# Optimization experiments

Measured on AMD Instinct MI355X. Metric: run time of the kernel, lower is better.

The kernel has to match this reference:

```python
import jax, jax.numpy as jnp
import numpy as np
from jax import lax

B, L, D = 2, 2048, 128
H, HD = 8, 32
WIN = 3

def setup_inputs() -> dict:
    key = jax.random.key(0)
    ks = jax.random.split(key, 7)
    s = 0.05
    return {
        "x":  jax.random.normal(ks[0], (B, L, D), jnp.float32),
        "pe": jax.random.normal(ks[1], (L, D), jnp.float32) * s,
        "Wq": jax.random.normal(ks[2], (D, H * HD), jnp.float32) * s,
        "bq": jnp.zeros((H * HD,), jnp.float32),
        "Wk": jax.random.normal(ks[3], (D, H * HD), jnp.float32) * s,
        "bk": jnp.zeros((H * HD,), jnp.float32),
        "Wv": jax.random.normal(ks[4], (D, H), jnp.float32) * s,
    }

def reference(x, pe, Wq, bq, Wk, bk, Wv):
    b, l, d = x.shape
    h = Wv.shape[1]
    hd = Wq.shape[1] // h
    xp = x + pe                                   # (B,L,D)
    # split heads: Dense output columns [i*hd:(i+1)*hd] -> head i
    q = (xp @ Wq + bq).reshape(b, l, h, hd).transpose(2, 0, 1, 3)  # (H,B,L,hd)
    k = (xp @ Wk + bk).reshape(b, l, h, hd).transpose(2, 0, 1, 3)  # (H,B,L,hd)
    v = jax.nn.sigmoid(x @ Wv).transpose(2, 0, 1)                  # (H,B,L)

    attn = jnp.einsum('hbqd,hbkd->hbqk', q, k) * (float(hd) ** -0.5)
    attn = jax.nn.softmax(attn, axis=-1)          # (H,B,L,L)

    # band_part(0,-1) + diag_part(k=(0,L-1)) (RIGHT_LEFT align) + transpose + reverse(-2,-1)
    # collapses to the skew-gather: R[p, m] = attn[L-1-p-m, L-1-p] for p+m <= L-1 else 0
    p = jnp.arange(l)[:, None]                    # (L,1)
    m = jnp.arange(l)[None, :]                    # (1,L)
    ii = l - 1 - p - m                            # row index  (L,L)
    jj = jnp.broadcast_to(l - 1 - p, (l, l))      # col index  (L,L)
    valid = (ii >= 0)
    R = attn[:, :, jnp.where(valid, ii, 0), jj] * valid.astype(attn.dtype)  # (H,B,L,L)

    R = R * v[:, :, :, None]                      # gate by value, broadcast over distance axis

    # TF avg_pool excludes padding from the divisor
    sums = lax.reduce_window(R, 0.0, lax.add, (1, 1, 1, WIN), (1, 1, 1, 1), 'SAME')
    cnt = lax.reduce_window(jnp.ones((l,), R.dtype), 0.0, lax.add, (WIN,), (1,), 'SAME')
    pooled = sums / cnt                           # (H,B,L,L)

    # global mode: sum over position axis, -> (B, L_dist, H)
    out = pooled.sum(axis=2).transpose(1, 2, 0)
    return out
```

## Files before the change

kernel.cpp:

```cpp
#include <hip/hip_runtime.h>
#include <hip/hip_bf16.h>

#define LSEQ 2048
#define BB 2
#define DD 128
#define HH 8
#define HD 32

#define FPSCALE 524288.0f
#define RFPSCALE (1.0f / 524288.0f)
#define DENSCALE 65536.0f
#define QSCALE 0.25503486f

typedef __bf16 bf8_t __attribute__((ext_vector_type(8)));
typedef __bf16 bf4_t __attribute__((ext_vector_type(4)));
typedef float f4_t __attribute__((ext_vector_type(4)));

__global__ __launch_bounds__(256) void k_A(const float* __restrict__ x,
                                           const float* __restrict__ pe,
                                           const float* __restrict__ Wq,
                                           const float* __restrict__ Wk,
                                           const float* __restrict__ Wv,
                                           const float* __restrict__ bq,
                                           const float* __restrict__ bk,
                                           float* __restrict__ w,
                                           __bf16* __restrict__ Qb,
                                           __bf16* __restrict__ Kb,
                                           int* __restrict__ Si,
                                           int* __restrict__ denI) {
    __shared__ __align__(16) char smem[34816];
    int gb = blockIdx.x;
    int tid = threadIdx.x;

    if (gb < 512) {
        __bf16* xs = (__bf16*)smem;
        __bf16* Wt = (__bf16*)(smem + 64 * 136 * 2);
        int jr = gb >> 3, y = gb & 7;
        int row0 = jr * 64;
        bool isK = y >= 4;
        int cbase = (y & 3) * 64;
        const float* W = isK ? Wk : Wq;

        #pragma unroll
        for (int i = 0; i < 8; i++) {
            int idx4 = tid + i * 256;
            int row = idx4 >> 5, col4 = idx4 & 31;
            float4 xv = ((const float4*)x)[row0 * 32 + idx4];
            float4 pv = ((const float4*)pe)[((row0 + row) & (LSEQ - 1)) * 32 + col4];
            bf4_t o = {(__bf16)(xv.x + pv.x), (__bf16)(xv.y + pv.y),
                       (__bf16)(xv.z + pv.z), (__bf16)(xv.w + pv.w)};
            *(bf4_t*)&xs[row * 136 + col4 * 4] = o;
        }
        #pragma unroll
        for (int i = 0; i < 8; i++) {
            int idx4 = tid + i * 256;
            int d = idx4 >> 4, c4 = (idx4 & 15) * 4;
            float4 wv4 = *(const float4*)(W + d * 256 + cbase + c4);
            Wt[(c4 + 0) * 136 + d] = (__bf16)wv4.x;
            Wt[(c4 + 1) * 136 + d] = (__bf16)wv4.y;
            Wt[(c4 + 2) * 136 + d] = (__bf16)wv4.z;
            Wt[(c4 + 3) * 136 + d] = (__bf16)wv4.w;
        }
        __syncthreads();

        int wid = tid >> 6, lane = tid & 63;
        int lm = lane & 15, lq = lane >> 4;
        int c0loc = wid * 16;
        f4_t acc0 = {0,0,0,0}, acc1 = {0,0,0,0}, acc2 = {0,0,0,0}, acc3 = {0,0,0,0};
        #pragma unroll
        for (int s = 0; s < 4; s++) {
            bf8_t bw = *(const bf8_t*)&Wt[(c0loc + lm) * 136 + lq * 8 + s * 32];
            bf8_t a0 = *(const bf8_t*)&xs[(0  + lm) * 136 + lq * 8 + s * 32];
            bf8_t a1 = *(const bf8_t*)&xs[(16 + lm) * 136 + lq * 8 + s * 32];
            bf8_t a2 = *(const bf8_t*)&xs[(32 + lm) * 136 + lq * 8 + s * 32];
            bf8_t a3 = *(const bf8_t*)&xs[(48 + lm) * 136 + lq * 8 + s * 32];
            acc0 = __builtin_amdgcn_mfma_f32_16x16x32_bf16(a0, bw, acc0, 0, 0, 0);
            acc1 = __builtin_amdgcn_mfma_f32_16x16x32_bf16(a1, bw, acc1, 0, 0, 0);
            acc2 = __builtin_amdgcn_mfma_f32_16x16x32_bf16(a2, bw, acc2, 0, 0, 0);
            acc3 = __builtin_amdgcn_mfma_f32_16x16x32_bf16(a3, bw, acc3, 0, 0, 0);
        }
        int c = cbase + c0loc + lm;
        float bv = (isK ? bk : bq)[c];
        float qs = isK ? 1.f : QSCALE;
        __bf16* Out = isK ? Kb : Qb;
        int h = c >> 5, hd = c & 31;
        f4_t accs[4] = {acc0, acc1, acc2, acc3};
        #pragma unroll
        for (int rs = 0; rs < 4; rs++) {
            #pragma unroll
            for (int r = 0; r < 4; r++) {
                int row = row0 + rs * 16 + lq * 4 + r;
                int b_ = row >> 11, l = row & (LSEQ - 1);
                Out[((h * BB + b_) * LSEQ + l) * HD + hd] =
                    (__bf16)((accs[rs][r] + bv) * qs);
            }
        }
    } else if (gb < 640) {
        float* xsf = (float*)smem;
        float* wvf = (float*)(smem + 32 * 132 * 4);
        int r0 = (gb - 512) * 32;
        for (int i = 0; i < 16; i++) {
            int idx = tid + i * 256;
            xsf[(idx >> 7) * 132 + (idx & 127)] = x[r0 * 128 + idx];
        }
        for (int i = 0; i < 4; i++) {
            int idx = tid + i * 256;
            wvf[idx] = Wv[idx];
        }
        __syncthreads();
        int rl = tid >> 3, h = tid & 7;
        float acc = 0.f;
        #pragma unroll 8
        for (int d = 0; d < 128; d++) acc += xsf[rl * 132 + d] * wvf[d * 8 + h];
        float sg = 1.f / (1.f + __expf(-acc));
        int r = r0 + rl;
        int b = r >> 11, l = r & (LSEQ - 1);
        w[(h * BB + b) * LSEQ + (LSEQ - 1 - l)] = sg;
    } else if (gb < 672) {
        int4 z = {0, 0, 0, 0};
        ((int4*)Si)[(gb - 640) * 256 + tid] = z;
    } else {
        int4 z = {0, 0, 0, 0};
        ((int4*)denI)[(gb - 672) * 256 + tid] = z;
    }
}

__global__ __launch_bounds__(256) void k_den(const __bf16* __restrict__ Qb,
                                             const __bf16* __restrict__ Kb,
                                             int* __restrict__ denI) {
    int hb = blockIdx.z;
    int q0 = blockIdx.y * 128;
    int kbase = blockIdx.x * 512;
    int wid = threadIdx.x >> 6, lane = threadIdx.x & 63;
    int lm = lane & 15, lq = lane >> 4;
    int qa = q0 + wid * 16;
    int qb2 = qa + 64;

    bf8_t aqa = *(const bf8_t*)(Qb + (hb * LSEQ + qa + lm) * HD + lq * 8);
    bf8_t aqb = *(const bf8_t*)(Qb + (hb * LSEQ + qb2 + lm) * HD + lq * 8);
    const __bf16* Khb = Kb + hb * LSEQ * HD;

    float dsa[4] = {0.f, 0.f, 0.f, 0.f};
    float dsb[4] = {0.f, 0.f, 0.f, 0.f};
    #pragma unroll 4
    for (int s = 0; s < 32; s++) {
        bf8_t bk_ = *(const bf8_t*)(Khb + (kbase + s * 16 + lm) * HD + lq * 8);
        f4_t z = {0.f, 0.f, 0.f, 0.f};
        f4_t sa = __builtin_amdgcn_mfma_f32_16x16x32_bf16(aqa, bk_, z, 0, 0, 0);
        f4_t sb = __builtin_amdgcn_mfma_f32_16x16x32_bf16(aqb, bk_, z, 0, 0, 0);
        #pragma unroll
        for (int r = 0; r < 4; r++) { dsa[r] += exp2f(sa[r]); dsb[r] += exp2f(sb[r]); }
    }
    #pragma unroll
    for (int r = 0; r < 4; r++) {
        float va = dsa[r], vb = dsb[r];
        va += __shfl_xor(va, 1); vb += __shfl_xor(vb, 1);
        va += __shfl_xor(va, 2); vb += __shfl_xor(vb, 2);
        va += __shfl_xor(va, 4); vb += __shfl_xor(vb, 4);
        va += __shfl_xor(va, 8); vb += __shfl_xor(vb, 8);
        dsa[r] = va; dsb[r] = vb;
    }
    if (lm == 0) {
        #pragma unroll
        for (int r = 0; r < 4; r++) {
            atomicAdd(&denI[hb * LSEQ + qa + lq * 4 + r],
                      __float2int_rn(dsa[r] * DENSCALE));
            atomicAdd(&denI[hb * LSEQ + qb2 + lq * 4 + r],
                      __float2int_rn(dsb[r] * DENSCALE));
        }
    }
}

#define SSTRIDE 332
__global__ __launch_bounds__(256) void k_scat(const __bf16* __restrict__ Qb,
                                              const __bf16* __restrict__ Kb,
                                              const float* __restrict__ w,
                                              const int* __restrict__ denI,
                                              int* __restrict__ S) {
    int hb = blockIdx.z;
    int q0 = blockIdx.y * 64;
    int kc0 = blockIdx.x * 256;
    if (kc0 + 256 <= q0) return;

    __shared__ int Sloc[16 * SSTRIDE];
    __shared__ float lwt[256];
    int tid = threadIdx.x;
    for (int i = tid; i < 16 * SSTRIDE; i += 256) Sloc[i] = 0;
    lwt[tid] = log2f(w[hb * LSEQ + kc0 + tid]);

    int wid = tid >> 6, lane = tid & 63;
    int lm = lane & 15, lq = lane >> 4;
    int qw0 = q0 + wid * 16;
    bf8_t aq = *(const bf8_t*)(Qb + (hb * LSEQ + qw0 + lm) * HD + lq * 8);
    float lrd[4];
    #pragma unroll
    for (int r = 0; r < 4; r++)
        lrd[r] = log2f(DENSCALE * FPSCALE / (float)denI[hb * LSEQ + qw0 + lq * 4 + r]);
    __syncthreads();

    const __bf16* Khb = Kb + hb * LSEQ * HD;
    int mbase = kc0 - q0 - 63;
    int qrow = qw0 + lq * 4;
    int* mySloc = Sloc + (wid * 4 + lq) * SSTRIDE;

    int sub_start = (qw0 > kc0) ? ((qw0 - kc0) >> 4) : 0;

    {
        int k0s = kc0 + sub_start * 16;
        bf8_t bk_ = *(const bf8_t*)(Khb + (k0s + lm) * HD + lq * 8);
        f4_t z = {0.f, 0.f, 0.f, 0.f};
        f4_t sc = __builtin_amdgcn_mfma_f32_16x16x32_bf16(aq, bk_, z, 0, 0, 0);
        float lw = lwt[sub_start * 16 + lm];
        int kcol = k0s + lm;
        #pragma unroll
        for (int r = 0; r < 4; r++) {
            int m = kcol - (qrow + r);
            if (m >= 0) {
                int iv = __float2int_rn(exp2f(sc[r] + lrd[r] + lw));
                atomicAdd(&mySloc[m - mbase], iv);
            }
        }
    }
    #pragma unroll 4
    for (int sub = sub_start + 1; sub < 16; sub++) {
        int k0s = kc0 + sub * 16;
        bf8_t bk_ = *(const bf8_t*)(Khb + (k0s + lm) * HD + lq * 8);
        f4_t z = {0.f, 0.f, 0.f, 0.f};
        f4_t sc = __builtin_amdgcn_mfma_f32_16x16x32_bf16(aq, bk_, z, 0, 0, 0);
        float lw = lwt[sub * 16 + lm];
        int kcol = k0s + lm;
        #pragma unroll
        for (int r = 0; r < 4; r++) {
            int m = kcol - (qrow + r);
            int iv = __float2int_rn(exp2f(sc[r] + lrd[r] + lw));
            atomicAdd(&mySloc[m - mbase], iv);
        }
    }
    __syncthreads();
    for (int i = tid; i < 320; i += 256) {
        int m = mbase + i;
        int v = 0;
        #pragma unroll
        for (int s = 0; s < 16; s++) v += Sloc[s * SSTRIDE + i];
        if (m >= 0 && m < LSEQ && v != 0)
            atomicAdd(&S[hb * LSEQ + m], v);
    }
}

__global__ __launch_bounds__(256) void k_out(const int* __restrict__ S,
                                             float* __restrict__ out) {
    int idx = blockIdx.x * 256 + threadIdx.x;
    int h = idx & 7;
    int m = (idx >> 3) & (LSEQ - 1);
    int b = idx >> 14;
    const int* Sr = S + (h * BB + b) * LSEQ;
    float s = (float)Sr[m];
    float cnt = 3.f;
    if (m > 0) s += (float)Sr[m - 1]; else cnt = 2.f;
    if (m < LSEQ - 1) s += (float)Sr[m + 1]; else cnt = 2.f;
    out[idx] = s * RFPSCALE / cnt;
}

extern "C" void kernel_launch(void* const* d_in, const int* in_sizes, int n_in,
                              void* d_out, int out_size, void* d_ws, size_t ws_size,
                              hipStream_t stream) {
    const float* x  = (const float*)d_in[0];
    const float* pe = (const float*)d_in[1];
    const float* Wq = (const float*)d_in[2];
    const float* bq = (const float*)d_in[3];
    const float* Wk = (const float*)d_in[4];
    const float* bk = (const float*)d_in[5];
    const float* Wv = (const float*)d_in[6];
    float* out = (float*)d_out;

    char* ws = (char*)d_ws;
    int*    Si   = (int*)(ws);
    float*  w    = (float*)(ws + 131072);
    __bf16* Qb   = (__bf16*)(ws + 262144);
    __bf16* Kb   = (__bf16*)(ws + 262144 + 2097152);
    int*    denI = (int*)(ws + 262144 + 4194304);

    k_A<<<704, 256, 0, stream>>>(x, pe, Wq, Wk, Wv, bq, bk, w, Qb, Kb, Si, denI);
    k_den<<<dim3(4, 16, 16), 256, 0, stream>>>(Qb, Kb, denI);
    k_scat<<<dim3(8, 32, 16), 256, 0, stream>>>(Qb, Kb, w, denI, Si);
    k_out<<<128, 256, 0, stream>>>(Si, out);
}
```

Before: 131.4 us.

## Fuse four kernels into one cooperative persistent kernel with grid syncs

```diff
diff --git a/kernel.cpp b/kernel.cpp
--- a/kernel.cpp
+++ b/kernel.cpp
@@ -1,5 +1,8 @@
 #include <hip/hip_runtime.h>
+#include <hip/hip_cooperative_groups.h>
 #include <hip/hip_bf16.h>
+
+namespace cg = cooperative_groups;
 
 #define LSEQ 2048
 #define BB 2
@@ -11,28 +14,27 @@
 #define RFPSCALE (1.0f / 524288.0f)
 #define DENSCALE 65536.0f
 #define QSCALE 0.25503486f
+#define SSTRIDE 332
 
 typedef __bf16 bf8_t __attribute__((ext_vector_type(8)));
 typedef __bf16 bf4_t __attribute__((ext_vector_type(4)));
 typedef float f4_t __attribute__((ext_vector_type(4)));
 
-__global__ __launch_bounds__(256) void k_A(const float* __restrict__ x,
-                                           const float* __restrict__ pe,
-                                           const float* __restrict__ Wq,
-                                           const float* __restrict__ Wk,
-                                           const float* __restrict__ Wv,
-                                           const float* __restrict__ bq,
-                                           const float* __restrict__ bk,
-                                           float* __restrict__ w,
-                                           __bf16* __restrict__ Qb,
-                                           __bf16* __restrict__ Kb,
-                                           int* __restrict__ Si,
-                                           int* __restrict__ denI) {
+__global__ __launch_bounds__(256, 2) void k_mega(
+        const float* __restrict__ x,  const float* __restrict__ pe,
+        const float* __restrict__ Wq, const float* __restrict__ Wk,
+        const float* __restrict__ Wv, const float* __restrict__ bq,
+        const float* __restrict__ bk,
+        float* __restrict__ w, __bf16* __restrict__ Qb, __bf16* __restrict__ Kb,
+        int* __restrict__ Si, int* __restrict__ denI, float* __restrict__ out) {
+    cg::grid_group grid = cg::this_grid();
     __shared__ __align__(16) char smem[34816];
     int gb = blockIdx.x;
     int tid = threadIdx.x;
-
-    if (gb < 512) {
+    int wid = tid >> 6, lane = tid & 63;
+    int lm = lane & 15, lq = lane >> 4;
+
+    {
         __bf16* xs = (__bf16*)smem;
         __bf16* Wt = (__bf16*)(smem + 64 * 136 * 2);
         int jr = gb >> 3, y = gb & 7;
@@ -63,8 +65,6 @@
         }
         __syncthreads();
 
-        int wid = tid >> 6, lane = tid & 63;
-        int lm = lane & 15, lq = lane >> 4;
         int c0loc = wid * 16;
         f4_t acc0 = {0,0,0,0}, acc1 = {0,0,0,0}, acc2 = {0,0,0,0}, acc3 = {0,0,0,0};
         #pragma unroll
@@ -95,10 +95,12 @@
                     (__bf16)((accs[rs][r] + bv) * qs);
             }
         }
-    } else if (gb < 640) {
+    }
+    if (gb < 128) {
+        __syncthreads();
         float* xsf = (float*)smem;
         float* wvf = (float*)(smem + 32 * 132 * 4);
-        int r0 = (gb - 512) * 32;
+        int r0 = gb * 32;
         for (int i = 0; i < 16; i++) {
             int idx = tid + i * 256;
             xsf[(idx >> 7) * 132 + (idx & 127)] = x[r0 * 128 + idx];
@@ -116,149 +118,148 @@
         int r = r0 + rl;
         int b = r >> 11, l = r & (LSEQ - 1);
         w[(h * BB + b) * LSEQ + (LSEQ - 1 - l)] = sg;
-    } else if (gb < 672) {
+    } else if (gb < 160) {
         int4 z = {0, 0, 0, 0};
-        ((int4*)Si)[(gb - 640) * 256 + tid] = z;
-    } else {
+        ((int4*)Si)[(gb - 128) * 256 + tid] = z;
+    } else if (gb < 192) {
         int4 z = {0, 0, 0, 0};
-        ((int4*)denI)[(gb - 672) * 256 + tid] = z;
-    }
-}
-
-__global__ __launch_bounds__(256) void k_den(const __bf16* __restrict__ Qb,
-                                             const __bf16* __restrict__ Kb,
-                                             int* __restrict__ denI) {
-    int hb = blockIdx.z;
-    int q0 = blockIdx.y * 128;
-    int kbase = blockIdx.x * 512;
-    int wid = threadIdx.x >> 6, lane = threadIdx.x & 63;
-    int lm = lane & 15, lq = lane >> 4;
-    int qa = q0 + wid * 16;
-    int qb2 = qa + 64;
-
-    bf8_t aqa = *(const bf8_t*)(Qb + (hb * LSEQ + qa + lm) * HD + lq * 8);
-    bf8_t aqb = *(const bf8_t*)(Qb + (hb * LSEQ + qb2 + lm) * HD + lq * 8);
-    const __bf16* Khb = Kb + hb * LSEQ * HD;
-
-    float dsa[4] = {0.f, 0.f, 0.f, 0.f};
-    float dsb[4] = {0.f, 0.f, 0.f, 0.f};
-    #pragma unroll 4
-    for (int s = 0; s < 32; s++) {
-        bf8_t bk_ = *(const bf8_t*)(Khb + (kbase + s * 16 + lm) * HD + lq * 8);
-        f4_t z = {0.f, 0.f, 0.f, 0.f};
-        f4_t sa = __builtin_amdgcn_mfma_f32_16x16x32_bf16(aqa, bk_, z, 0, 0, 0);
-        f4_t sb = __builtin_amdgcn_mfma_f32_16x16x32_bf16(aqb, bk_, z, 0, 0, 0);
-        #pragma unroll
-        for (int r = 0; r < 4; r++) { dsa[r] += exp2f(sa[r]); dsb[r] += exp2f(sb[r]); }
-    }
+        ((int4*)denI)[(gb - 160) * 256 + tid] = z;
+    }
+    grid.sync();
+
     #pragma unroll
-    for (int r = 0; r < 4; r++) {
-        float va = dsa[r], vb = dsb[r];
-        va += __shfl_xor(va, 1); vb += __shfl_xor(vb, 1);
-        va += __shfl_xor(va, 2); vb += __shfl_xor(vb, 2);
-        va += __shfl_xor(va, 4); vb += __shfl_xor(vb, 4);
-        va += __shfl_xor(va, 8); vb += __shfl_xor(vb, 8);
-        dsa[r] = va; dsb[r] = vb;
-    }
-    if (lm == 0) {
+    for (int j = 0; j < 2; j++) {
+        int u = gb + j * 512;
+        int hb = u >> 6;
+        int rem = u & 63;
+        int q0 = (rem >> 2) * 128;
+        int kbase = (rem & 3) * 512;
+        int qa = q0 + wid * 16;
+        int qb2 = qa + 64;
+
+        bf8_t aqa = *(const bf8_t*)(Qb + (hb * LSEQ + qa + lm) * HD + lq * 8);
+        bf8_t aqb = *(const bf8_t*)(Qb + (hb * LSEQ + qb2 + lm) * HD + lq * 8);
+        const __bf16* Khb = Kb + hb * LSEQ * HD;
+
+        float dsa[4] = {0.f, 0.f, 0.f, 0.f};
+        float dsb[4] = {0.f, 0.f, 0.f, 0.f};
+        #pragma unroll 4
+        for (int s = 0; s < 32; s++) {
+            bf8_t bk_ = *(const bf8_t*)(Khb + (kbase + s * 16 + lm) * HD + lq * 8);
+            f4_t z = {0.f, 0.f, 0.f, 0.f};
+            f4_t sa = __builtin_amdgcn_mfma_f32_16x16x32_bf16(aqa, bk_, z, 0, 0, 0);
+            f4_t sb = __builtin_amdgcn_mfma_f32_16x16x32_bf16(aqb, bk_, z, 0, 0, 0);
+            #pragma unroll
+            for (int r = 0; r < 4; r++) { dsa[r] += exp2f(sa[r]); dsb[r] += exp2f(sb[r]); }
+        }
         #pragma unroll
         for (int r = 0; r < 4; r++) {
-            atomicAdd(&denI[hb * LSEQ + qa + lq * 4 + r],
-                      __float2int_rn(dsa[r] * DENSCALE));
-            atomicAdd(&denI[hb * LSEQ + qb2 + lq * 4 + r],
-                      __float2int_rn(dsb[r] * DENSCALE));
-        }
-    }
-}
-
-#define SSTRIDE 332
-__global__ __launch_bounds__(256) void k_scat(const __bf16* __restrict__ Qb,
-                                              const __bf16* __restrict__ Kb,
-                                              const float* __restrict__ w,
-                                              const int* __restrict__ denI,
-                                              int* __restrict__ S) {
-    int hb = blockIdx.z;
-    int q0 = blockIdx.y * 64;
-    int kc0 = blockIdx.x * 256;
-    if (kc0 + 256 <= q0) return;
-
-    __shared__ int Sloc[16 * SSTRIDE];
-    __shared__ float lwt[256];
-    int tid = threadIdx.x;
-    for (int i = tid; i < 16 * SSTRIDE; i += 256) Sloc[i] = 0;
-    lwt[tid] = log2f(w[hb * LSEQ + kc0 + tid]);
-
-    int wid = tid >> 6, lane = tid & 63;
-    int lm = lane & 15, lq = lane >> 4;
-    int qw0 = q0 + wid * 16;
-    bf8_t aq = *(const bf8_t*)(Qb + (hb * LSEQ + qw0 + lm) * HD + lq * 8);
-    float lrd[4];
-    #pragma unroll
-    for (int r = 0; r < 4; r++)
-        lrd[r] = log2f(DENSCALE * FPSCALE / (float)denI[hb * LSEQ + qw0 + lq * 4 + r]);
-    __syncthreads();
-
-    const __bf16* Khb = Kb + hb * LSEQ * HD;
-    int mbase = kc0 - q0 - 63;
-    int qrow = qw0 + lq * 4;
-    int* mySloc = Sloc + (wid * 4 + lq) * SSTRIDE;
-
-    int sub_start = (qw0 > kc0) ? ((qw0 - kc0) >> 4) : 0;
+            float va = dsa[r], vb = dsb[r];
+            va += __shfl_xor(va, 1); vb += __shfl_xor(vb, 1);
+            va += __shfl_xor(va, 2); vb += __shfl_xor(vb, 2);
+            va += __shfl_xor(va, 4); vb += __shfl_xor(vb, 4);
+            va += __shfl_xor(va, 8); vb += __shfl_xor(vb, 8);
+            dsa[r] = va; dsb[r] = vb;
+        }
+        if (lm == 0) {
+            #pragma unroll
+            for (int r = 0; r < 4; r++) {
+                atomicAdd(&denI[hb * LSEQ + qa + lq * 4 + r],
+                          __float2int_rn(dsa[r] * DENSCALE));
+                atomicAdd(&denI[hb * LSEQ + qb2 + lq * 4 + r],
+                          __float2int_rn(dsb[r] * DENSCALE));
+            }
+        }
+    }
+    grid.sync();
 
     {
-        int k0s = kc0 + sub_start * 16;
-        bf8_t bk_ = *(const bf8_t*)(Khb + (k0s + lm) * HD + lq * 8);
-        f4_t z = {0.f, 0.f, 0.f, 0.f};
-        f4_t sc = __builtin_amdgcn_mfma_f32_16x16x32_bf16(aq, bk_, z, 0, 0, 0);
-        float lw = lwt[sub_start * 16 + lm];
-        int kcol = k0s + lm;
-        #pragma unroll
-        for (int r = 0; r < 4; r++) {
-            int m = kcol - (qrow + r);
-            if (m >= 0) {
-                int iv = __float2int_rn(exp2f(sc[r] + lrd[r] + lw));
-                atomicAdd(&mySloc[m - mbase], iv);
-            }
-        }
-    }
-    #pragma unroll 4
-    for (int sub = sub_start + 1; sub < 16; sub++) {
-        int k0s = kc0 + sub * 16;
-        bf8_t bk_ = *(const bf8_t*)(Khb + (k0s + lm) * HD + lq * 8);
-        f4_t z = {0.f, 0.f, 0.f, 0.f};
-        f4_t sc = __builtin_amdgcn_mfma_f32_16x16x32_bf16(aq, bk_, z, 0, 0, 0);
-        float lw = lwt[sub * 16 + lm];
-        int kcol = k0s + lm;
-        #pragma unroll
-        for (int r = 0; r < 4; r++) {
-            int m = kcol - (qrow + r);
-            int iv = __float2int_rn(exp2f(sc[r] + lrd[r] + lw));
-            atomicAdd(&mySloc[m - mbase], iv);
-        }
-    }
-    __syncthreads();
-    for (int i = tid; i < 320; i += 256) {
-        int m = mbase + i;
-        int v = 0;
-        #pragma unroll
-        for (int s = 0; s < 16; s++) v += Sloc[s * SSTRIDE + i];
-        if (m >= 0 && m < LSEQ && v != 0)
-            atomicAdd(&S[hb * LSEQ + m], v);
-    }
-}
-
-__global__ __launch_bounds__(256) void k_out(const int* __restrict__ S,
-                                             float* __restrict__ out) {
-    int idx = blockIdx.x * 256 + threadIdx.x;
-    int h = idx & 7;
-    int m = (idx >> 3) & (LSEQ - 1);
-    int b = idx >> 14;
-    const int* Sr = S + (h * BB + b) * LSEQ;
-    float s = (float)Sr[m];
-    float cnt = 3.f;
-    if (m > 0) s += (float)Sr[m - 1]; else cnt = 2.f;
-    if (m < LSEQ - 1) s += (float)Sr[m + 1]; else cnt = 2.f;
-    out[idx] = s * RFPSCALE / cnt;
+        int* Sloc = (int*)smem;
+        float* lwt = (float*)(smem + 16 * SSTRIDE * 4);
+        for (int t = gb; t < 2304; t += 512) {
+            int hb = t / 144;
+            int s = t - hb * 144;
+            int kc = 0;
+            while (2 * (kc + 1) * (kc + 2) <= s) kc++;
+            int q0i = s - 2 * kc * (kc + 1);
+            int q0 = q0i * 64;
+            int kc0 = kc * 256;
+
+            for (int i = tid; i < 16 * SSTRIDE; i += 256) Sloc[i] = 0;
+            lwt[tid] = log2f(w[hb * LSEQ + kc0 + tid]);
+
+            int qw0 = q0 + wid * 16;
+            bf8_t aq = *(const bf8_t*)(Qb + (hb * LSEQ + qw0 + lm) * HD + lq * 8);
+            float lrd[4];
+            #pragma unroll
+            for (int r = 0; r < 4; r++)
+                lrd[r] = log2f(DENSCALE * FPSCALE /
+                               (float)denI[hb * LSEQ + qw0 + lq * 4 + r]);
+            __syncthreads();
+
+            const __bf16* Khb = Kb + hb * LSEQ * HD;
+            int mbase = kc0 - q0 - 63;
+            int qrow = qw0 + lq * 4;
+            int* mySloc = Sloc + (wid * 4 + lq) * SSTRIDE;
+            int sub_start = (qw0 > kc0) ? ((qw0 - kc0) >> 4) : 0;
+
+            {
+                int k0s = kc0 + sub_start * 16;
+                bf8_t bk_ = *(const bf8_t*)(Khb + (k0s + lm) * HD + lq * 8);
+                f4_t z = {0.f, 0.f, 0.f, 0.f};
+                f4_t sc = __builtin_amdgcn_mfma_f32_16x16x32_bf16(aq, bk_, z, 0, 0, 0);
+                float lw = lwt[sub_start * 16 + lm];
+                int kcol = k0s + lm;
+                #pragma unroll
+                for (int r = 0; r < 4; r++) {
+                    int m = kcol - (qrow + r);
+                    if (m >= 0) {
+                        int iv = __float2int_rn(exp2f(sc[r] + lrd[r] + lw));
+                        atomicAdd(&mySloc[m - mbase], iv);
+                    }
+                }
+            }
+            #pragma unroll 4
+            for (int sub = sub_start + 1; sub < 16; sub++) {
+                int k0s = kc0 + sub * 16;
+                bf8_t bk_ = *(const bf8_t*)(Khb + (k0s + lm) * HD + lq * 8);
+                f4_t z = {0.f, 0.f, 0.f, 0.f};
+                f4_t sc = __builtin_amdgcn_mfma_f32_16x16x32_bf16(aq, bk_, z, 0, 0, 0);
+                float lw = lwt[sub * 16 + lm];
+                int kcol = k0s + lm;
+                #pragma unroll
+                for (int r = 0; r < 4; r++) {
+                    int m = kcol - (qrow + r);
+                    int iv = __float2int_rn(exp2f(sc[r] + lrd[r] + lw));
+                    atomicAdd(&mySloc[m - mbase], iv);
+                }
+            }
+            __syncthreads();
+            for (int i = tid; i < 320; i += 256) {
+                int m = mbase + i;
+                int v = 0;
+                #pragma unroll
+                for (int sl = 0; sl < 16; sl++) v += Sloc[sl * SSTRIDE + i];
+                if (m >= 0 && m < LSEQ && v != 0)
+                    atomicAdd(&Si[hb * LSEQ + m], v);
+            }
+            __syncthreads();
+        }
+    }
+    grid.sync();
+
+    if (gb < 128) {
+        int idx = gb * 256 + tid;
+        int h = idx & 7;
+        int m = (idx >> 3) & (LSEQ - 1);
+        int b = idx >> 14;
+        const int* Sr = Si + (h * BB + b) * LSEQ;
+        float s = (float)Sr[m];
+        float cnt = 3.f;
+        if (m > 0) s += (float)Sr[m - 1]; else cnt = 2.f;
+        if (m < LSEQ - 1) s += (float)Sr[m + 1]; else cnt = 2.f;
+        out[idx] = s * RFPSCALE / cnt;
+    }
 }
 
 extern "C" void kernel_launch(void* const* d_in, const int* in_sizes, int n_in,
@@ -280,8 +281,8 @@
     __bf16* Kb   = (__bf16*)(ws + 262144 + 2097152);
     int*    denI = (int*)(ws + 262144 + 4194304);
 
-    k_A<<<704, 256, 0, stream>>>(x, pe, Wq, Wk, Wv, bq, bk, w, Qb, Kb, Si, denI);
-    k_den<<<dim3(4, 16, 16), 256, 0, stream>>>(Qb, Kb, denI);
-    k_scat<<<dim3(8, 32, 16), 256, 0, stream>>>(Qb, Kb, w, denI, Si);
-    k_out<<<128, 256, 0, stream>>>(Si, out);
+    void* args[] = {(void*)&x, (void*)&pe, (void*)&Wq, (void*)&Wk, (void*)&Wv,
+                    (void*)&bq, (void*)&bk, (void*)&w, (void*)&Qb, (void*)&Kb,
+                    (void*)&Si, (void*)&denI, (void*)&out};
+    hipLaunchCooperativeKernel((void*)k_mega, dim3(512), dim3(256), args, 0, stream);
 }
```

New measurement: 308.8 us. +135.0%, slower.
